# Optimization experiments

Hardware: AMD Instinct MI355X
Metric: run time of the kernel (lower is better)

Reference implementation:

```python
import jax, jax.numpy as jnp
import numpy as np

B, SQ, SK, HID, H, D = 2, 2048, 2048, 1024, 16, 64
LN_EPS = 1e-12


def _sinusoid(seq_len):
    # [1,1,S,D]: first half sin, second half cos (RoFormer convention)
    pos = np.arange(seq_len, dtype=np.float32)[:, None]
    inv_freq = 1.0 / (10000.0 ** (np.arange(0, D, 2, dtype=np.float32) / D))
    ang = pos * inv_freq  # [S, D/2]
    return jnp.asarray(np.concatenate([np.sin(ang), np.cos(ang)], axis=-1)[None, None], dtype=jnp.float32)


def setup_inputs() -> dict:
    key = jax.random.key(0)
    ks = jax.random.split(key, 12)
    w = lambda k, shape: jax.random.normal(k, shape, dtype=jnp.float32) * 0.02
    return {
        "hidden_states": jax.random.normal(ks[0], (B, SQ, HID), dtype=jnp.float32),
        "encoder_hidden_states": jax.random.normal(ks[1], (B, SK, HID), dtype=jnp.float32),
        "encoder_attention_mask": jnp.zeros((B, 1, 1, SK), dtype=jnp.float32),  # additive mask
        "sinusoidal_pos": _sinusoid(SQ),
        "c_sinusoidal_pos": _sinusoid(SK),
        "Wq": w(ks[2], (HID, HID)), "bq": jnp.zeros((HID,), jnp.float32),
        "Wk": w(ks[3], (HID, HID)), "bk": jnp.zeros((HID,), jnp.float32),
        "Wv": w(ks[4], (HID, HID)), "bv": jnp.zeros((HID,), jnp.float32),
        "Wd": w(ks[5], (HID, HID)), "bd": jnp.zeros((HID,), jnp.float32),
        "ln_gamma": jnp.ones((HID,), jnp.float32),
        "ln_beta": jnp.zeros((HID,), jnp.float32),
    }


def apply_rope(sinusoidal_pos, layer):
    # sinusoidal_pos: [1,1,S,D] = sin||cos halves; layer: [B,H,S,D]
    sin, cos = jnp.split(sinusoidal_pos, 2, axis=-1)
    sin_pos = jnp.stack([sin, sin], axis=-1).reshape(sinusoidal_pos.shape)
    cos_pos = jnp.stack([cos, cos], axis=-1).reshape(sinusoidal_pos.shape)
    rot = jnp.stack([-layer[..., 1::2], layer[..., ::2]], axis=-1).reshape(layer.shape)
    return layer * cos_pos + rot * sin_pos


def _heads(x):
    b, s, _ = x.shape
    return x.reshape(b, s, H, D).transpose(0, 2, 1, 3)  # [B,H,S,D]


def reference(hidden_states, encoder_hidden_states, encoder_attention_mask,
              sinusoidal_pos, c_sinusoidal_pos,
              Wq, bq, Wk, bk, Wv, bv, Wd, bd, ln_gamma, ln_beta):
    q = _heads(hidden_states @ Wq.T + bq)
    k = _heads(encoder_hidden_states @ Wk.T + bk)
    v = _heads(encoder_hidden_states @ Wv.T + bv)
    q = apply_rope(sinusoidal_pos, q)
    k = apply_rope(c_sinusoidal_pos, k)

    scores = jnp.einsum("bhqd,bhkd->bhqk", q, k) / jnp.sqrt(jnp.float32(D))
    scores = scores + encoder_attention_mask  # broadcast [B,1,1,SK]
    probs = jax.nn.softmax(scores, axis=-1)
    ctx = jnp.einsum("bhqk,bhkd->bhqd", probs, v)
    ctx = ctx.transpose(0, 2, 1, 3).reshape(hidden_states.shape[0], -1, HID)

    proj = ctx @ Wd.T + bd
    x = hidden_states + proj
    mu = jnp.mean(x, axis=-1, keepdims=True)
    var = jnp.mean(jnp.square(x - mu), axis=-1, keepdims=True)
    return (x - mu) / jnp.sqrt(var + LN_EPS) * ln_gamma + ln_beta
```

## Files before the change

### kernel.cpp

```cpp
#include <hip/hip_runtime.h>

typedef __attribute__((ext_vector_type(8))) short short8;
typedef __attribute__((ext_vector_type(4))) float f32x4;
typedef __attribute__((ext_vector_type(16))) float f32x16;

#define LOG2E 1.4426950408889634f
#define QSCALE 0.18033688011112042f

#define ASM_VMCNT2() asm volatile("s_waitcnt vmcnt(2)" ::: "memory")
#define ASM_VMCNT0() asm volatile("s_waitcnt vmcnt(0)" ::: "memory")
#define ASM_LGKM0()  asm volatile("s_waitcnt lgkmcnt(0)" ::: "memory")

static __device__ __forceinline__ unsigned short f2bf(float f){
  unsigned u = __builtin_bit_cast(unsigned, f);
  u += 0x7FFFu + ((u>>16)&1u);
  return (unsigned short)(u>>16);
}

static __device__ __forceinline__ void async16(const void* g, const void* l){
  __builtin_amdgcn_global_load_lds(
      (const __attribute__((address_space(1))) unsigned*)(unsigned long long)g,
      (__attribute__((address_space(3))) unsigned*)(unsigned)(unsigned long long)l,
      16, 0, 0);
}

__global__ __launch_bounds__(256) void prep_kernel(
    const float* __restrict__ hidden, unsigned short* __restrict__ hb,
    const float* __restrict__ encoder, unsigned short* __restrict__ eb,
    const float* __restrict__ Wq, unsigned short* __restrict__ wqb,
    const float* __restrict__ Wk, unsigned short* __restrict__ wkb,
    const float* __restrict__ Wv, unsigned short* __restrict__ wvb,
    const float* __restrict__ Wd, unsigned short* __restrict__ wdb,
    const float* __restrict__ mask, float* __restrict__ maskE)
{
  int blk = blockIdx.x;
  if (blk < 6144){
    const float* src; unsigned short* dst; int i;
    if (blk < 4096){
      int t = blk*256 + threadIdx.x;
      src = (t >> 19) ? encoder : hidden;
      dst = (t >> 19) ? eb : hb;
      i = (t & 524287)*8;
    } else {
      int t = (blk-4096)*256 + threadIdx.x;
      int z = t >> 17;
      src = (z==0)?Wq:(z==1)?Wk:(z==2)?Wv:Wd;
      dst = (z==0)?wqb:(z==1)?wkb:(z==2)?wvb:wdb;
      i = (t & 131071)*8;
    }
    const float4* s4 = (const float4*)(src + i);
    float4 a = s4[0], b = s4[1];
    union { unsigned short u[8]; short8 v; } o;
    o.u[0]=f2bf(a.x); o.u[1]=f2bf(a.y); o.u[2]=f2bf(a.z); o.u[3]=f2bf(a.w);
    o.u[4]=f2bf(b.x); o.u[5]=f2bf(b.y); o.u[6]=f2bf(b.z); o.u[7]=f2bf(b.w);
    *(short8*)(dst + i) = o.v;
  } else {
    int i = (blk-6144)*256 + threadIdx.x;
    float4 v = ((const float4*)mask)[i];
    v.x*=LOG2E; v.y*=LOG2E; v.z*=LOG2E; v.w*=LOG2E;
    ((float4*)maskE)[i] = v;
  }
}

__global__ __launch_bounds__(512) void gemm_qkv(
    const unsigned short* __restrict__ hb, const unsigned short* __restrict__ eb,
    const unsigned short* __restrict__ wqb, const unsigned short* __restrict__ wkb,
    const unsigned short* __restrict__ wvb,
    const float* __restrict__ bq, const float* __restrict__ bk, const float* __restrict__ bv,
    const float* __restrict__ sp, const float* __restrict__ csp,
    unsigned short* __restrict__ Qb, unsigned short* __restrict__ Kb, unsigned short* __restrict__ Vt)
{
  const int flat = blockIdx.x;
  const int work = (flat&7)*96 + (flat>>3);
  const int bn  = work & 7;
  const int zbm = work >> 3;
  const int z  = zbm >> 5;
  const int bm = zbm & 31;

  const unsigned short* A = (z==0) ? hb : eb;
  const unsigned short* W = (z==0) ? wqb : (z==1 ? wkb : wvb);
  const float* bias = (z==0) ? bq : (z==1 ? bk : bv);
  const float* rope = (z==0) ? sp : (z==1 ? csp : nullptr);

  __shared__ unsigned short As[2][128*32];
  __shared__ unsigned short Bs[2][128*32];

  const int tid = threadIdx.x;
  const int w = tid>>6, l = tid&63;
  const int wr = w>>1, wc = w&1;
  const int srow = tid>>2, scol = (tid&3)*8;

  const f32x4 zero = {0.f,0.f,0.f,0.f};
  f32x4 acc[2][4];
  #pragma unroll
  for (int mi=0;mi<2;mi++)
    #pragma unroll
    for (int ni=0;ni<4;ni++) acc[mi][ni] = zero;

  auto stage = [&](int buf, int kt){
    async16(A + (size_t)(bm*128 + srow)*1024 + kt*32 + scol, As[buf] + tid*8);
    async16(W + (size_t)(bn*128 + srow)*1024 + kt*32 + scol, Bs[buf] + tid*8);
  };

  stage(0, 0);

  for (int kt=0; kt<32; ++kt){
    int cur = kt&1;
    if (kt < 31){ stage(cur^1, kt+1); ASM_VMCNT2(); }
    else        { ASM_VMCNT0(); }
    __builtin_amdgcn_s_barrier();
    __builtin_amdgcn_sched_barrier(0);

    short8 af[2], bf[4];
    #pragma unroll
    for (int mi=0;mi<2;mi++)
      af[mi] = *(const short8*)(As[cur] + (wr*32 + mi*16 + (l&15))*32 + (l>>4)*8);
    #pragma unroll
    for (int ni=0;ni<4;ni++)
      bf[ni] = *(const short8*)(Bs[cur] + (wc*64 + ni*16 + (l&15))*32 + (l>>4)*8);
    #pragma unroll
    for (int mi=0;mi<2;mi++)
      #pragma unroll
      for (int ni=0;ni<4;ni++)
        acc[mi][ni] = __builtin_amdgcn_mfma_f32_16x16x32_bf16(af[mi], bf[ni], acc[mi][ni], 0,0,0);

    ASM_LGKM0();
    __builtin_amdgcn_s_barrier();
  }

  if (z == 2){
    #pragma unroll
    for (int mi=0;mi<2;mi++){
      #pragma unroll
      for (int ni=0;ni<4;ni++){
        int mr0 = bm*128 + wr*32 + mi*16 + (l>>4)*4;
        int nc  = bn*128 + wc*64 + ni*16 + (l&15);
        int b0 = mr0>>11, s0 = mr0&2047;
        int h = nc>>6, d = nc&63;
        float bia = bias[nc];
        union { unsigned short u[4]; unsigned long long ull; } pk;
        #pragma unroll
        for (int r=0;r<4;r++) pk.u[r] = f2bf(acc[mi][ni][r] + bia);
        *(unsigned long long*)(Vt + ((size_t)(b0*16 + h)*64 + d)*2048 + s0) = pk.ull;
      }
    }
  } else {
    #pragma unroll
    for (int mi=0;mi<2;mi++){
      #pragma unroll
      for (int ni=0;ni<4;ni++){
        #pragma unroll
        for (int r=0;r<4;r++){
          int mr = bm*128 + wr*32 + mi*16 + (l>>4)*4 + r;
          int nc = bn*128 + wc*64 + ni*16 + (l&15);
          float v = acc[mi][ni][r] + bias[nc];
          int b = mr>>11, s = mr&2047;
          int h = nc>>6,  d = nc&63;
          float p = __shfl_xor(v, 1);
          float sv = rope[s*64 + (d>>1)];
          float cv = rope[s*64 + 32 + (d>>1)];
          float ov = (d&1) ? (v*cv + p*sv) : (v*cv - p*sv);
          if (z == 0) ov *= QSCALE;
          unsigned short* out = (z==0) ? Qb : Kb;
          out[((size_t)(b*16 + h)*2048 + s)*64 + d] = f2bf(ov);
        }
      }
    }
  }
}

__global__ __launch_bounds__(512) void flash_attn(
    const unsigned short* __restrict__ Qb, const unsigned short* __restrict__ Kb,
    const unsigned short* __restrict__ Vt, const float* __restrict__ maskE,
    unsigned short* __restrict__ ctx)
{
  __shared__ unsigned short Kls[2][2][4096];
  __shared__ unsigned short Vls[2][2][4096];
  __shared__ float maskLS[2048];

  const int tid = threadIdx.x;
  const int w = tid>>6, l = tid&63;
  const int qc = l&31, hi = l>>5;
  const int wq = w&3, half = w>>2;

  const int flat = blockIdx.x;
  const int o = (flat&7)*64 + (flat>>3);
  const int qt = o&15, bh = o>>4;
  const int b = bh>>4, h = bh&15;

  {
    ((float4*)maskLS)[tid] = ((const float4*)(maskE + b*2048))[tid];
  }

  const int qrow = qt*128 + wq*32 + qc;
  const unsigned short* qptr = Qb + ((size_t)bh*2048 + qrow)*64;
  short8 qf[4];
  #pragma unroll
  for (int ks=0;ks<4;ks++) qf[ks] = *(const short8*)(qptr + ks*16 + hi*8);

  short8 onesf;
  #pragma unroll
  for (int i=0;i<8;i++) onesf[i] = (short)0x3F80;

  f32x16 oacc[2], lacc;
  #pragma unroll
  for (int t3=0;t3<2;t3++)
    #pragma unroll
    for (int i=0;i<16;i++) oacc[t3][i] = 0.f;
  #pragma unroll
  for (int i=0;i<16;i++) lacc[i] = 0.f;

  const int srow = l>>3;
  const int scol = ((l&7) ^ srow)*8;
  const unsigned short* kSrc0; const unsigned short* kSrc1;
  const unsigned short* vSrc0; const unsigned short* vSrc1;
  {
    int c0 = wq*2, c1 = wq*2+1;
    kSrc0 = Kb + ((size_t)bh*2048 + half*1024 + c0*8 + srow)*64 + scol;
    kSrc1 = Kb + ((size_t)bh*2048 + half*1024 + c1*8 + srow)*64 + scol;
    vSrc0 = Vt + ((size_t)bh*64 + c0*8 + srow)*2048 + half*1024 + scol;
    vSrc1 = Vt + ((size_t)bh*64 + c1*8 + srow)*2048 + half*1024 + scol;
  }
  const int ld0 = (wq*2)*512 + l*8, ld1 = (wq*2+1)*512 + l*8;

  auto stage = [&](int buf){
    async16(kSrc0, &Kls[half][buf][ld0]);
    async16(kSrc1, &Kls[half][buf][ld1]);
    async16(vSrc0, &Vls[half][buf][ld0]);
    async16(vSrc1, &Vls[half][buf][ld1]);
    kSrc0 += 4096; kSrc1 += 4096;
    vSrc0 += 64;   vSrc1 += 64;
  };

  stage(0);
  __syncthreads();
  int cur = 0;

  const int rg0 = (qc&7);

  for (int ktl=0; ktl<16; ++ktl){
    if (ktl < 15) stage(cur^1);

    f32x16 sacc[2];
    #pragma unroll
    for (int t2=0;t2<2;t2++){
      #pragma unroll
      for (int rg=0;rg<4;rg++){
        const float4 mv = *(const float4*)&maskLS[half*1024 + ktl*64 + t2*32 + rg*8 + hi*4];
        sacc[t2][rg*4+0] = mv.x;
        sacc[t2][rg*4+1] = mv.y;
        sacc[t2][rg*4+2] = mv.z;
        sacc[t2][rg*4+3] = mv.w;
      }
    }

    __builtin_amdgcn_s_setprio(1);
    #pragma unroll
    for (int ks=0; ks<4; ++ks){
      const short8 kf0 = *(const short8*)(&Kls[half][cur][ qc*64      + (((ks*2+hi)^rg0)*8) ]);
      const short8 kf1 = *(const short8*)(&Kls[half][cur][ (32+qc)*64 + (((ks*2+hi)^rg0)*8) ]);
      sacc[0] = __builtin_amdgcn_mfma_f32_32x32x16_bf16(kf0, qf[ks], sacc[0], 0,0,0);
      sacc[1] = __builtin_amdgcn_mfma_f32_32x32x16_bf16(kf1, qf[ks], sacc[1], 0,0,0);
    }
    __builtin_amdgcn_s_setprio(0);

    #pragma unroll
    for (int t2=0;t2<2;t2++)
      #pragma unroll
      for (int i=0;i<16;i++)
        sacc[t2][i] = __builtin_amdgcn_exp2f(sacc[t2][i]);

    short8 pB[4];
    #pragma unroll
    for (int t2=0;t2<2;t2++){
      #pragma unroll
      for (int hf=0; hf<2; ++hf){
        unsigned x0,x1,x2,x3;
        asm("v_cvt_pk_bf16_f32 %0, %1, %2" : "=v"(x0) : "v"(sacc[t2][hf*8+0]), "v"(sacc[t2][hf*8+1]));
        asm("v_cvt_pk_bf16_f32 %0, %1, %2" : "=v"(x1) : "v"(sacc[t2][hf*8+2]), "v"(sacc[t2][hf*8+3]));
        asm("v_cvt_pk_bf16_f32 %0, %1, %2" : "=v"(x2) : "v"(sacc[t2][hf*8+4]), "v"(sacc[t2][hf*8+5]));
        asm("v_cvt_pk_bf16_f32 %0, %1, %2" : "=v"(x3) : "v"(sacc[t2][hf*8+6]), "v"(sacc[t2][hf*8+7]));
        asm("v_permlane32_swap_b32 %0, %1" : "+v"(x2), "+v"(x0));
        asm("v_permlane32_swap_b32 %0, %1" : "+v"(x3), "+v"(x1));
        union { unsigned u[4]; short8 v; } pb;
        pb.u[0]=x0; pb.u[1]=x1; pb.u[2]=x2; pb.u[3]=x3;
        pB[t2*2+hf] = pb.v;
      }
    }

    __builtin_amdgcn_s_setprio(1);
    #pragma unroll
    for (int t3=0;t3<2;t3++){
      #pragma unroll
      for (int si=0; si<4; ++si){
        const short8 vf = *(const short8*)(&Vls[half][cur][ (t3*32+qc)*64 + (((si*2+hi)^rg0)*8) ]);
        oacc[t3] = __builtin_amdgcn_mfma_f32_32x32x16_bf16(vf, pB[si], oacc[t3], 0,0,0);
      }
    }
    #pragma unroll
    for (int si=0; si<4; ++si)
      lacc = __builtin_amdgcn_mfma_f32_32x32x16_bf16(onesf, pB[si], lacc, 0,0,0);
    __builtin_amdgcn_s_setprio(0);

    __syncthreads();
    cur ^= 1;
  }

  float l_r = lacc[0];

  float* Ox  = (float*)&Kls[0][0][0];
  float* Lf  = (float*)&Vls[0][0][0];

  if (half == 1){
    #pragma unroll
    for (int t3=0;t3<2;t3++){
      #pragma unroll
      for (int rg=0;rg<4;rg++){
        int dbase = t3*32 + rg*8 + hi*4;
        f32x4 o4 = { oacc[t3][rg*4+0], oacc[t3][rg*4+1], oacc[t3][rg*4+2], oacc[t3][rg*4+3] };
        *(f32x4*)&Ox[wq*2048 + qc*64 + (dbase ^ (rg0*8))] = o4;
      }
    }
    if (hi == 0) Lf[wq*32 + qc] = l_r;
  }
  __syncthreads();

  if (half == 0){
    float l1 = Lf[wq*32 + qc];
    float inv = 1.0f / (l_r + l1);

    int qglob = qt*128 + wq*32 + qc;
    unsigned short* cp = ctx + ((size_t)b*2048 + qglob)*1024 + h*64;
    #pragma unroll
    for (int t3=0;t3<2;t3++){
      #pragma unroll
      for (int rg=0;rg<4;rg++){
        int dbase = t3*32 + rg*8 + hi*4;
        f32x4 o1 = *(const f32x4*)&Ox[wq*2048 + qc*64 + (dbase ^ (rg0*8))];
        union { unsigned short u[4]; unsigned long long ull; } pk4;
        #pragma unroll
        for (int i=0;i<4;i++) pk4.u[i] = f2bf((oacc[t3][rg*4+i] + o1[i])*inv);
        *(unsigned long long*)(cp + dbase) = pk4.ull;
      }
    }
  }
}

__global__ __launch_bounds__(512) void gemm_proj(
    const unsigned short* __restrict__ ctxb, const unsigned short* __restrict__ wdb,
    const float* __restrict__ bd, const float* __restrict__ hidden,
    float* __restrict__ X)
{
  const int flat = blockIdx.x;
  const int work = (flat&7)*32 + (flat>>3);
  const int bn = work & 7;
  const int bm = work >> 3;

  __shared__ unsigned short As[2][128*32];
  __shared__ unsigned short Bs[2][128*32];
  const int tid = threadIdx.x;
  const int w = tid>>6, l = tid&63;
  const int wr = w>>1, wc = w&1;
  const int srow = tid>>2, scol = (tid&3)*8;

  const f32x4 zero = {0.f,0.f,0.f,0.f};
  f32x4 acc[2][4];
  #pragma unroll
  for (int mi=0;mi<2;mi++)
    #pragma unroll
    for (int ni=0;ni<4;ni++) acc[mi][ni] = zero;

  auto stage = [&](int buf, int kt){
    async16(ctxb + (size_t)(bm*128 + srow)*1024 + kt*32 + scol, As[buf] + tid*8);
    async16(wdb  + (size_t)(bn*128 + srow)*1024 + kt*32 + scol, Bs[buf] + tid*8);
  };

  stage(0, 0);

  for (int kt=0; kt<32; ++kt){
    int cur = kt&1;
    if (kt < 31){ stage(cur^1, kt+1); ASM_VMCNT2(); }
    else        { ASM_VMCNT0(); }
    __builtin_amdgcn_s_barrier();
    __builtin_amdgcn_sched_barrier(0);

    short8 af[2], bf[4];
    #pragma unroll
    for (int mi=0;mi<2;mi++)
      af[mi] = *(const short8*)(As[cur] + (wr*32 + mi*16 + (l&15))*32 + (l>>4)*8);
    #pragma unroll
    for (int ni=0;ni<4;ni++)
      bf[ni] = *(const short8*)(Bs[cur] + (wc*64 + ni*16 + (l&15))*32 + (l>>4)*8);
    #pragma unroll
    for (int mi=0;mi<2;mi++)
      #pragma unroll
      for (int ni=0;ni<4;ni++)
        acc[mi][ni] = __builtin_amdgcn_mfma_f32_16x16x32_bf16(af[mi], bf[ni], acc[mi][ni], 0,0,0);

    ASM_LGKM0();
    __builtin_amdgcn_s_barrier();
  }

  #pragma unroll
  for (int mi=0;mi<2;mi++){
    #pragma unroll
    for (int ni=0;ni<4;ni++){
      #pragma unroll
      for (int r=0;r<4;r++){
        int mr = bm*128 + wr*32 + mi*16 + (l>>4)*4 + r;
        int nc = bn*128 + wc*64 + ni*16 + (l&15);
        float v = acc[mi][ni][r] + bd[nc] + hidden[(size_t)mr*1024 + nc];
        X[(size_t)mr*1024 + nc] = v;
      }
    }
  }
}

__global__ __launch_bounds__(256) void ln_kernel(
    const float* __restrict__ X, const float* __restrict__ gamma,
    const float* __restrict__ beta, float* __restrict__ out)
{
  const int row = blockIdx.x;
  const int tid = threadIdx.x;
  const float4 v = ((const float4*)(X + (size_t)row*1024))[tid];
  float s  = v.x+v.y+v.z+v.w;
  float ss = v.x*v.x + v.y*v.y + v.z*v.z + v.w*v.w;
  #pragma unroll
  for (int off=1; off<64; off<<=1){
    s  += __shfl_xor(s, off);
    ss += __shfl_xor(ss, off);
  }
  __shared__ float red[8];
  const int w = tid>>6, l = tid&63;
  if (l == 0){ red[w] = s; red[4+w] = ss; }
  __syncthreads();
  s  = red[0]+red[1]+red[2]+red[3];
  ss = red[4]+red[5]+red[6]+red[7];
  float mu  = s*(1.f/1024.f);
  float var = ss*(1.f/1024.f) - mu*mu;
  float inv = rsqrtf(var + 1e-12f);
  const float4 g  = ((const float4*)gamma)[tid];
  const float4 bt = ((const float4*)beta)[tid];
  float4 o;
  o.x = (v.x-mu)*inv*g.x + bt.x;
  o.y = (v.y-mu)*inv*g.y + bt.y;
  o.z = (v.z-mu)*inv*g.z + bt.z;
  o.w = (v.w-mu)*inv*g.w + bt.w;
  ((float4*)(out + (size_t)row*1024))[tid] = o;
}

extern "C" void kernel_launch(void* const* d_in, const int* in_sizes, int n_in,
                              void* d_out, int out_size, void* d_ws, size_t ws_size,
                              hipStream_t stream) {
  const float* hidden  = (const float*)d_in[0];
  const float* encoder = (const float*)d_in[1];
  const float* mask    = (const float*)d_in[2];
  const float* sp      = (const float*)d_in[3];
  const float* csp     = (const float*)d_in[4];
  const float* Wq = (const float*)d_in[5];  const float* bq = (const float*)d_in[6];
  const float* Wk = (const float*)d_in[7];  const float* bk = (const float*)d_in[8];
  const float* Wv = (const float*)d_in[9];  const float* bv = (const float*)d_in[10];
  const float* Wd = (const float*)d_in[11]; const float* bd = (const float*)d_in[12];
  const float* gamma = (const float*)d_in[13];
  const float* beta  = (const float*)d_in[14];

  char* ws = (char*)d_ws;
  const size_t MB_ = 1ull<<20;
  unsigned short* hb  = (unsigned short*)(ws + 0);
  unsigned short* eb  = (unsigned short*)(ws + 8*MB_);
  unsigned short* wqb = (unsigned short*)(ws + 16*MB_);
  unsigned short* wkb = (unsigned short*)(ws + 18*MB_);
  unsigned short* wvb = (unsigned short*)(ws + 20*MB_);
  unsigned short* wdb = (unsigned short*)(ws + 22*MB_);
  unsigned short* Qb  = (unsigned short*)(ws + 24*MB_);
  unsigned short* Kb  = (unsigned short*)(ws + 32*MB_);
  unsigned short* Vt  = (unsigned short*)(ws + 40*MB_);
  unsigned short* ctxb = hb;
  float* X = (float*)(ws + 24*MB_);
  float* maskE = (float*)(ws + 48*MB_);

  prep_kernel<<<6148,256,0,stream>>>(hidden, hb, encoder, eb,
                                     Wq, wqb, Wk, wkb, Wv, wvb, Wd, wdb,
                                     mask, maskE);

  gemm_qkv<<<768,512,0,stream>>>(hb, eb, wqb, wkb, wvb,
                                 bq, bk, bv, sp, csp, Qb, Kb, Vt);
  flash_attn<<<512,512,0,stream>>>(Qb, Kb, Vt, maskE, ctxb);
  gemm_proj<<<256,512,0,stream>>>(ctxb, wdb, bd, hidden, X);
  ln_kernel<<<4096,256,0,stream>>>(X, gamma, beta, (float*)d_out);
}
```

Baseline: 127.9 us.

## Replace ones-MFMA row sum with lazy-max softmax; halve proj GEMM M-tile

In flash attention, the row-sum MFMA against a ones matrix is replaced by summing the exponentials in VALU with a cross-half permlane swap. A lazy running max is added that rescales only when a row sum would overflow, and the two K-halves are merged with max-aware scaling. Separately, the projection GEMM tile is cut from 128x128 to 64x128 and the grid doubled to 512 blocks, to fill more CUs. The change drops four MFMAs per iteration but adds VALU reductions and a rarely taken rescale branch, and the smaller proj tile lowers data reuse per block.

```diff
diff --git a/kernel.cpp b/kernel.cpp
--- a/kernel.cpp
+++ b/kernel.cpp
@@ -8,6 +8,7 @@
 #define QSCALE 0.18033688011112042f
 
 #define ASM_VMCNT2() asm volatile("s_waitcnt vmcnt(2)" ::: "memory")
+#define ASM_VMCNT1() asm volatile("s_waitcnt vmcnt(1)" ::: "memory")
 #define ASM_VMCNT0() asm volatile("s_waitcnt vmcnt(0)" ::: "memory")
 #define ASM_LGKM0()  asm volatile("s_waitcnt lgkmcnt(0)" ::: "memory")
 
@@ -198,17 +199,12 @@
   #pragma unroll
   for (int ks=0;ks<4;ks++) qf[ks] = *(const short8*)(qptr + ks*16 + hi*8);
 
-  short8 onesf;
-  #pragma unroll
-  for (int i=0;i<8;i++) onesf[i] = (short)0x3F80;
-
-  f32x16 oacc[2], lacc;
+  float m_r = 0.f, l_r = 0.f;
+  f32x16 oacc[2];
   #pragma unroll
   for (int t3=0;t3<2;t3++)
     #pragma unroll
     for (int i=0;i<16;i++) oacc[t3][i] = 0.f;
-  #pragma unroll
-  for (int i=0;i<16;i++) lacc[i] = 0.f;
 
   const int srow = l>>3;
   const int scol = ((l&7) ^ srow)*8;
@@ -264,11 +260,42 @@
     }
     __builtin_amdgcn_s_setprio(0);
 
+    float rs = 0.f;
     #pragma unroll
     for (int t2=0;t2<2;t2++)
       #pragma unroll
-      for (int i=0;i<16;i++)
-        sacc[t2][i] = __builtin_amdgcn_exp2f(sacc[t2][i]);
+      for (int i=0;i<16;i++){
+        float e = __builtin_amdgcn_exp2f(sacc[t2][i] - m_r);
+        sacc[t2][i] = e;
+        rs += e;
+      }
+    { float a = rs, c2 = rs;
+      asm("v_permlane32_swap_b32 %0, %1" : "+v"(a), "+v"(c2));
+      rs = a + c2; }
+
+    if (__builtin_expect(!__all(rs <= 16777216.0f), 0)){
+      float cm = 1.0f;
+      #pragma unroll
+      for (int t2=0;t2<2;t2++)
+        #pragma unroll
+        for (int i=0;i<16;i++) cm = fmaxf(cm, sacc[t2][i]);
+      { float a = cm, c2 = cm;
+        asm("v_permlane32_swap_b32 %0, %1" : "+v"(a), "+v"(c2));
+        cm = fmaxf(a, c2); }
+      float rin = 1.0f/cm;
+      #pragma unroll
+      for (int t2=0;t2<2;t2++)
+        #pragma unroll
+        for (int i=0;i<16;i++) sacc[t2][i] *= rin;
+      #pragma unroll
+      for (int t3=0;t3<2;t3++)
+        #pragma unroll
+        for (int i=0;i<16;i++) oacc[t3][i] *= rin;
+      l_r *= rin;
+      rs  *= rin;
+      m_r += log2f(cm);
+    }
+    l_r += rs;
 
     short8 pB[4];
     #pragma unroll
@@ -297,19 +324,14 @@
         oacc[t3] = __builtin_amdgcn_mfma_f32_32x32x16_bf16(vf, pB[si], oacc[t3], 0,0,0);
       }
     }
-    #pragma unroll
-    for (int si=0; si<4; ++si)
-      lacc = __builtin_amdgcn_mfma_f32_32x32x16_bf16(onesf, pB[si], lacc, 0,0,0);
     __builtin_amdgcn_s_setprio(0);
 
     __syncthreads();
     cur ^= 1;
   }
 
-  float l_r = lacc[0];
-
   float* Ox  = (float*)&Kls[0][0][0];
-  float* Lf  = (float*)&Vls[0][0][0];
+  float* MLf = (float*)&Vls[0][0][0];
 
   if (half == 1){
     #pragma unroll
@@ -321,13 +343,21 @@
         *(f32x4*)&Ox[wq*2048 + qc*64 + (dbase ^ (rg0*8))] = o4;
       }
     }
-    if (hi == 0) Lf[wq*32 + qc] = l_r;
+    if (hi == 0){
+      MLf[wq*64 + qc]      = m_r;
+      MLf[wq*64 + 32 + qc] = l_r;
+    }
   }
   __syncthreads();
 
   if (half == 0){
-    float l1 = Lf[wq*32 + qc];
-    float inv = 1.0f / (l_r + l1);
+    float m1 = MLf[wq*64 + qc];
+    float l1 = MLf[wq*64 + 32 + qc];
+    float mstar = fmaxf(m_r, m1);
+    float s0 = __builtin_amdgcn_exp2f(m_r - mstar);
+    float s1 = __builtin_amdgcn_exp2f(m1 - mstar);
+    float inv = 1.0f / (l_r*s0 + l1*s1);
+    float a0 = s0*inv, a1 = s1*inv;
 
     int qglob = qt*128 + wq*32 + qc;
     unsigned short* cp = ctx + ((size_t)b*2048 + qglob)*1024 + h*64;
@@ -339,7 +369,7 @@
         f32x4 o1 = *(const f32x4*)&Ox[wq*2048 + qc*64 + (dbase ^ (rg0*8))];
         union { unsigned short u[4]; unsigned long long ull; } pk4;
         #pragma unroll
-        for (int i=0;i<4;i++) pk4.u[i] = f2bf((oacc[t3][rg*4+i] + o1[i])*inv);
+        for (int i=0;i<4;i++) pk4.u[i] = f2bf(oacc[t3][rg*4+i]*a0 + o1[i]*a1);
         *(unsigned long long*)(cp + dbase) = pk4.ull;
       }
     }
@@ -352,49 +382,53 @@
     float* __restrict__ X)
 {
   const int flat = blockIdx.x;
-  const int work = (flat&7)*32 + (flat>>3);
+  const int work = (flat&7)*64 + (flat>>3);
   const int bn = work & 7;
   const int bm = work >> 3;
 
-  __shared__ unsigned short As[2][128*32];
+  __shared__ unsigned short As[2][64*32];
   __shared__ unsigned short Bs[2][128*32];
   const int tid = threadIdx.x;
   const int w = tid>>6, l = tid&63;
-  const int wr = w>>1, wc = w&1;
-  const int srow = tid>>2, scol = (tid&3)*8;
+  const int wr = w>>2, wc = w&3;
 
   const f32x4 zero = {0.f,0.f,0.f,0.f};
-  f32x4 acc[2][4];
+  f32x4 acc[2][2];
   #pragma unroll
   for (int mi=0;mi<2;mi++)
     #pragma unroll
-    for (int ni=0;ni<4;ni++) acc[mi][ni] = zero;
+    for (int ni=0;ni<2;ni++) acc[mi][ni] = zero;
 
   auto stage = [&](int buf, int kt){
-    async16(ctxb + (size_t)(bm*128 + srow)*1024 + kt*32 + scol, As[buf] + tid*8);
-    async16(wdb  + (size_t)(bn*128 + srow)*1024 + kt*32 + scol, Bs[buf] + tid*8);
+    if (tid < 256)
+      async16(ctxb + (size_t)(bm*64 + (tid>>2))*1024 + kt*32 + (tid&3)*8, As[buf] + tid*8);
+    async16(wdb + (size_t)(bn*128 + (tid>>2))*1024 + kt*32 + (tid&3)*8, Bs[buf] + tid*8);
   };
 
   stage(0, 0);
 
   for (int kt=0; kt<32; ++kt){
     int cur = kt&1;
-    if (kt < 31){ stage(cur^1, kt+1); ASM_VMCNT2(); }
-    else        { ASM_VMCNT0(); }
+    if (kt < 31){
+      stage(cur^1, kt+1);
+      if (w < 4) ASM_VMCNT2(); else ASM_VMCNT1();
+    } else {
+      ASM_VMCNT0();
+    }
     __builtin_amdgcn_s_barrier();
     __builtin_amdgcn_sched_barrier(0);
 
-    short8 af[2], bf[4];
+    short8 af[2], bf[2];
     #pragma unroll
     for (int mi=0;mi<2;mi++)
       af[mi] = *(const short8*)(As[cur] + (wr*32 + mi*16 + (l&15))*32 + (l>>4)*8);
     #pragma unroll
-    for (int ni=0;ni<4;ni++)
-      bf[ni] = *(const short8*)(Bs[cur] + (wc*64 + ni*16 + (l&15))*32 + (l>>4)*8);
+    for (int ni=0;ni<2;ni++)
+      bf[ni] = *(const short8*)(Bs[cur] + (wc*32 + ni*16 + (l&15))*32 + (l>>4)*8);
     #pragma unroll
     for (int mi=0;mi<2;mi++)
       #pragma unroll
-      for (int ni=0;ni<4;ni++)
+      for (int ni=0;ni<2;ni++)
         acc[mi][ni] = __builtin_amdgcn_mfma_f32_16x16x32_bf16(af[mi], bf[ni], acc[mi][ni], 0,0,0);
 
     ASM_LGKM0();
@@ -404,11 +438,11 @@
   #pragma unroll
   for (int mi=0;mi<2;mi++){
     #pragma unroll
-    for (int ni=0;ni<4;ni++){
+    for (int ni=0;ni<2;ni++){
       #pragma unroll
       for (int r=0;r<4;r++){
-        int mr = bm*128 + wr*32 + mi*16 + (l>>4)*4 + r;
-        int nc = bn*128 + wc*64 + ni*16 + (l&15);
+        int mr = bm*64 + wr*32 + mi*16 + (l>>4)*4 + r;
+        int nc = bn*128 + wc*32 + ni*16 + (l&15);
         float v = acc[mi][ni][r] + bd[nc] + hidden[(size_t)mr*1024 + nc];
         X[(size_t)mr*1024 + nc] = v;
       }
@@ -486,6 +520,6 @@
   gemm_qkv<<<768,512,0,stream>>>(hb, eb, wqb, wkb, wvb,
                                  bq, bk, bv, sp, csp, Qb, Kb, Vt);
   flash_attn<<<512,512,0,stream>>>(Qb, Kb, Vt, maskE, ctxb);
-  gemm_proj<<<256,512,0,stream>>>(ctxb, wdb, bd, hidden, X);
+  gemm_proj<<<512,512,0,stream>>>(ctxb, wdb, bd, hidden, X);
   ln_kernel<<<4096,256,0,stream>>>(X, gamma, beta, (float*)d_out);
 }
```

Measured after the change: 123.0 us. 1.04x faster.
